# Optimization experiments

Hardware: AMD Instinct MI355X
Metric: run time of the kernel (lower is better)

Reference implementation:

```python
import jax, jax.numpy as jnp
import numpy as np

B, N_E, E_DIM = 131072, 1024, 64
BETA = 0.25


def setup_inputs() -> dict:
    key = jax.random.key(0)
    kz, kw = jax.random.split(key)
    z = jax.random.normal(kz, (B, E_DIM), dtype=jnp.float32)
    # nn.Embedding init: uniform(-1/n_e, 1/n_e)
    emb_w = jax.random.uniform(kw, (N_E, E_DIM), dtype=jnp.float32,
                               minval=-1.0 / N_E, maxval=1.0 / N_E)
    return {"z": z, "emb_w": emb_w}


def reference(z, emb_w):
    beta = jnp.float32(BETA)
    # pairwise squared distances: [B, n_e]
    d = (jnp.sum(z * z, axis=1, keepdims=True)
         + jnp.sum(emb_w * emb_w, axis=1)
         - 2.0 * jnp.einsum('bd,nd->bn', z, emb_w))
    idx = jnp.argmin(d, axis=1)                      # [B]
    z_q = jnp.take(emb_w, idx, axis=0)               # [B, e_dim]
    # legacy=False branch
    loss = (beta * jnp.mean((jax.lax.stop_gradient(z_q) - z) ** 2)
            + jnp.mean((z_q - jax.lax.stop_gradient(z)) ** 2))
    # straight-through estimator
    z_q_st = z + jax.lax.stop_gradient(z_q - z)
    # torch.var is unbiased (ddof=1)
    v = jnp.var(idx.astype(jnp.float32), ddof=1)
    return (z_q_st, loss, idx, v)
```

## Files before the change

### kernel.cpp

```cpp
#include <hip/hip_runtime.h>
#include <stdint.h>


typedef __attribute__((ext_vector_type(8))) __bf16 bf16x8;
typedef __attribute__((ext_vector_type(4))) float f32x4;

#define OUT_LOSS 8388608
#define OUT_IDX  8388609
#define OUT_VAR  8519681

#define WS_LOSS  0
#define WS_S1    4096
#define WS_S2    8192
#define WS_EFRAG 12288
#define WS_EE    143360

__device__ __forceinline__ void gld_lds16(const void* g, void* l) {
  __builtin_amdgcn_global_load_lds(
      (const __attribute__((address_space(1))) unsigned*)g,
      (__attribute__((address_space(3))) unsigned*)l, 16, 0, 0);
}

__global__ void vq_prep(const float* __restrict__ emb, char* __restrict__ ws) {
  bf16x8* efrag = (bf16x8*)(ws + WS_EFRAG);
  float* eeoff = (float*)(ws + WS_EE);
  const int t = blockIdx.x;
  const int l = threadIdx.x;
  const int n = t * 16 + (l & 15);
  const int kb0 = (l >> 4) * 8;
  const float* er = emb + n * 64;
  for (int j = 0; j < 2; ++j) {
    const int kb = j * 32 + kb0;
    bf16x8 h;
#pragma unroll
    for (int i = 0; i < 8; ++i) h[i] = (__bf16)(-2.0f * er[kb + i]);
    efrag[(t * 2 + j) * 64 + l] = h;
  }
  if (l < 16) {
    const float* e2 = emb + (t * 16 + l) * 64;
    float s = 0.f;
#pragma unroll
    for (int d = 0; d < 64; ++d) s += e2[d] * e2[d];
    eeoff[t * 16 + l] = s + 0.5f;
  }
}

__global__ void __launch_bounds__(256) vq_main(
    const float* __restrict__ z, const float* __restrict__ emb,
    float* __restrict__ out, char* __restrict__ ws) {
  __shared__ char smfrag[16384];
  __shared__ float see[1024];
  __shared__ float sL[4];
  __shared__ int sA[4], sB[4];

  const int tid = threadIdx.x;
  const int wave = tid >> 6, lane = tid & 63;
  const int lr = lane & 15, ksl = lane >> 4;
  const int k0 = ksl * 8;
  const int row_base = blockIdx.x * 128 + wave * 32;

  gld_lds16(ws + WS_EE + wave * 1024 + lane * 16, (char*)see + wave * 1024);
#pragma unroll
  for (int i = 0; i < 4; ++i)
    gld_lds16(ws + WS_EFRAG + i * 4096 + wave * 1024 + lane * 16,
              smfrag + i * 4096 + wave * 1024);

  bf16x8 zfa0, zfa1, zfb0, zfb1;
  float zza, zzb;
  {
    const float* zra = z + (size_t)(row_base + lr) * 64;
    const float* zrb = z + (size_t)(row_base + 16 + lr) * 64;
    f32x4 a0 = *(const f32x4*)(zra + k0);
    f32x4 a1 = *(const f32x4*)(zra + k0 + 4);
    f32x4 a2 = *(const f32x4*)(zra + 32 + k0);
    f32x4 a3 = *(const f32x4*)(zra + 32 + k0 + 4);
    f32x4 b0 = *(const f32x4*)(zrb + k0);
    f32x4 b1 = *(const f32x4*)(zrb + k0 + 4);
    f32x4 b2 = *(const f32x4*)(zrb + 32 + k0);
    f32x4 b3 = *(const f32x4*)(zrb + 32 + k0 + 4);
    float sa = 0.f, sb = 0.f;
#pragma unroll
    for (int i = 0; i < 4; ++i) {
      zfa0[i] = (__bf16)a0[i]; zfa0[4 + i] = (__bf16)a1[i];
      zfa1[i] = (__bf16)a2[i]; zfa1[4 + i] = (__bf16)a3[i];
      zfb0[i] = (__bf16)b0[i]; zfb0[4 + i] = (__bf16)b1[i];
      zfb1[i] = (__bf16)b2[i]; zfb1[4 + i] = (__bf16)b3[i];
      sa += a0[i] * a0[i] + a1[i] * a1[i] + a2[i] * a2[i] + a3[i] * a3[i];
      sb += b0[i] * b0[i] + b1[i] * b1[i] + b2[i] * b2[i] + b3[i] * b3[i];
    }
    sa += __shfl_xor(sa, 16, 64); sa += __shfl_xor(sa, 32, 64);
    sb += __shfl_xor(sb, 16, 64); sb += __shfl_xor(sb, 32, 64);
    zza = sa; zzb = sb;
  }

  unsigned rka = 0xFFFFFFFFu, rkb = 0xFFFFFFFFu;
  const unsigned k4 = (unsigned)(ksl * 4);
  const bf16x8* sfrag = (const bf16x8*)smfrag;

  for (int ph = 0; ph < 8; ++ph) {
    __syncthreads();
#pragma unroll
    for (int tt = 0; tt < 8; ++tt) {
      const int g = ph * 8 + tt;
      bf16x8 e0 = sfrag[(tt * 2 + 0) * 64 + lane];
      bf16x8 e1 = sfrag[(tt * 2 + 1) * 64 + lane];
      const f32x4 ee = *(const f32x4*)(see + g * 16 + ksl * 4);
      f32x4 a = __builtin_amdgcn_mfma_f32_16x16x32_bf16(e0, zfa0, ee, 0, 0, 0);
      a = __builtin_amdgcn_mfma_f32_16x16x32_bf16(e1, zfa1, a, 0, 0, 0);
      f32x4 b = __builtin_amdgcn_mfma_f32_16x16x32_bf16(e0, zfb0, ee, 0, 0, 0);
      b = __builtin_amdgcn_mfma_f32_16x16x32_bf16(e1, zfb1, b, 0, 0, 0);
      const unsigned tw = (unsigned)(g * 16);
      {
        const unsigned t0 = (__float_as_uint(a[0]) & 0xFFFFFC00u) | (k4 + 0);
        const unsigned t1 = (__float_as_uint(a[1]) & 0xFFFFFC00u) | (k4 + 1);
        const unsigned t2 = (__float_as_uint(a[2]) & 0xFFFFFC00u) | (k4 + 2);
        const unsigned t3 = (__float_as_uint(a[3]) & 0xFFFFFC00u) | (k4 + 3);
        rka = min(rka, min(min(t0, t1), min(t2, t3)) + tw);
      }
      {
        const unsigned t0 = (__float_as_uint(b[0]) & 0xFFFFFC00u) | (k4 + 0);
        const unsigned t1 = (__float_as_uint(b[1]) & 0xFFFFFC00u) | (k4 + 1);
        const unsigned t2 = (__float_as_uint(b[2]) & 0xFFFFFC00u) | (k4 + 2);
        const unsigned t3 = (__float_as_uint(b[3]) & 0xFFFFFC00u) | (k4 + 3);
        rkb = min(rkb, min(min(t0, t1), min(t2, t3)) + tw);
      }
    }
    __syncthreads();
    if (ph < 7) {
#pragma unroll
      for (int i = 0; i < 4; ++i)
        gld_lds16(ws + WS_EFRAG + (ph + 1) * 16384 + i * 4096 + wave * 1024 + lane * 16,
                  smfrag + i * 4096 + wave * 1024);
    }
  }

  rka = min(rka, (unsigned)__shfl_xor((int)rka, 16, 64));
  rka = min(rka, (unsigned)__shfl_xor((int)rka, 32, 64));
  rkb = min(rkb, (unsigned)__shfl_xor((int)rkb, 16, 64));
  rkb = min(rkb, (unsigned)__shfl_xor((int)rkb, 32, 64));

  const int erow = lane >> 1, eseg = lane & 1;
  const int src = erow & 15;
  const unsigned ka = (unsigned)__shfl((int)rka, src, 64);
  const unsigned kb = (unsigned)__shfl((int)rkb, src, 64);
  const float za = __shfl(zza, src, 64);
  const float zb = __shfl(zzb, src, 64);
  const unsigned k = (erow < 16) ? ka : kb;
  const float zzv = (erow < 16) ? za : zb;
  const unsigned idx = k & 1023u;
  const size_t rowg = (size_t)row_base + erow;
  const f32x4* ep = (const f32x4*)(emb + (size_t)idx * 64 + eseg * 32);
  f32x4* op = (f32x4*)(out + rowg * 64 + eseg * 32);
#pragma unroll
  for (int c = 0; c < 8; ++c) op[c] = ep[c];

  float ls = 0.f; int s1 = 0, s2 = 0;
  if (eseg == 0) {
    ls = zzv + __uint_as_float(k & 0xFFFFFC00u) - 0.5f;
    s1 = (int)idx;
    s2 = (int)(idx * idx);
    out[OUT_IDX + rowg] = (float)idx;
  }
#pragma unroll
  for (int off = 1; off < 64; off <<= 1) {
    ls += __shfl_xor(ls, off, 64);
    s1 += __shfl_xor(s1, off, 64);
    s2 += __shfl_xor(s2, off, 64);
  }
  if (lane == 0) { sL[wave] = ls; sA[wave] = s1; sB[wave] = s2; }
  __syncthreads();
  if (tid == 0) {
    float L = 0; int a = 0, b = 0;
#pragma unroll
    for (int w = 0; w < 4; ++w) { L += sL[w]; a += sA[w]; b += sB[w]; }
    ((float*)(ws + WS_LOSS))[blockIdx.x] = L;
    ((int*)(ws + WS_S1))[blockIdx.x] = a;
    ((int*)(ws + WS_S2))[blockIdx.x] = b;
  }
}

__global__ void vq_final(float* __restrict__ out, const char* __restrict__ ws) {
  const int t = threadIdx.x;
  const float* lp = (const float*)(ws + WS_LOSS);
  const int* p1 = (const int*)(ws + WS_S1);
  const int* p2 = (const int*)(ws + WS_S2);
  double L = 0; long long a = 0, b = 0;
#pragma unroll
  for (int kk = 0; kk < 4; ++kk) {
    const int i = t + 256 * kk;
    L += (double)lp[i];
    a += (long long)p1[i];
    b += (long long)p2[i];
  }
#pragma unroll
  for (int off = 1; off < 64; off <<= 1) {
    L += __shfl_xor(L, off, 64);
    a += __shfl_xor(a, off, 64);
    b += __shfl_xor(b, off, 64);
  }
  __shared__ double sL[4];
  __shared__ long long sA[4], sB[4];
  const int wave = t >> 6, lane = t & 63;
  if (lane == 0) { sL[wave] = L; sA[wave] = a; sB[wave] = b; }
  __syncthreads();
  if (t == 0) {
    double Lt = 0; long long at = 0, bt = 0;
#pragma unroll
    for (int w = 0; w < 4; ++w) { Lt += sL[w]; at += sA[w]; bt += sB[w]; }
    out[OUT_LOSS] = (float)(1.25 * Lt / 8388608.0);
    long long num = bt * 131072LL - at * at;
    out[OUT_VAR] = (float)((double)num / (131072.0 * 131071.0));
  }
}

extern "C" void kernel_launch(void* const* d_in, const int* in_sizes, int n_in,
                              void* d_out, int out_size, void* d_ws, size_t ws_size,
                              hipStream_t stream) {
  (void)in_sizes; (void)n_in; (void)out_size; (void)ws_size;
  const float* z = (const float*)d_in[0];
  const float* emb = (const float*)d_in[1];
  float* out = (float*)d_out;
  char* ws = (char*)d_ws;
  vq_prep<<<64, 64, 0, stream>>>(emb, ws);
  vq_main<<<1024, 256, 0, stream>>>(z, emb, out, ws);
  vq_final<<<1, 256, 0, stream>>>(out, ws);
}
```

Measured before the change: 46.89 us.

## Double-buffer codebook fragments in LDS with explicit vmcnt waits

Splits the LDS fragment buffer into two halves and prefetches the next phase's codebook fragments while the current phase is being computed. Explicit s_waitcnt vmcnt plus raw s_barrier replace the __syncthreads pairs, and the phase loop is fully unrolled. The intent is to hide global-to-LDS load latency behind MFMA work. It also swaps an add for an OR when merging the tile offset into the packed key, which is valid because the low bits are disjoint. The cost is twice the LDS footprint, which may reduce occupancy, and hand-counted vmcnt values that depend on how many loads the compiler has in flight.

Result: faster. 45.70 us (-2.6%).

```diff
diff --git a/kernel.cpp b/kernel.cpp
--- a/kernel.cpp
+++ b/kernel.cpp
@@ -48,7 +48,7 @@
 __global__ void __launch_bounds__(256) vq_main(
     const float* __restrict__ z, const float* __restrict__ emb,
     float* __restrict__ out, char* __restrict__ ws) {
-  __shared__ char smfrag[16384];
+  __shared__ char smfrag[2][16384];
   __shared__ float see[1024];
   __shared__ float sL[4];
   __shared__ int sA[4], sB[4];
@@ -59,11 +59,17 @@
   const int k0 = ksl * 8;
   const int row_base = blockIdx.x * 128 + wave * 32;
 
+#define STAGE(ph, buf)                                                         \
+  {                                                                            \
+    _Pragma("unroll")                                                          \
+    for (int i_ = 0; i_ < 4; ++i_)                                             \
+      gld_lds16(ws + WS_EFRAG + (ph) * 16384 + i_ * 4096 + wave * 1024 + lane * 16, \
+                smfrag[buf] + i_ * 4096 + wave * 1024);                        \
+  }
+
   gld_lds16(ws + WS_EE + wave * 1024 + lane * 16, (char*)see + wave * 1024);
-#pragma unroll
-  for (int i = 0; i < 4; ++i)
-    gld_lds16(ws + WS_EFRAG + i * 4096 + wave * 1024 + lane * 16,
-              smfrag + i * 4096 + wave * 1024);
+  STAGE(0, 0);
+  STAGE(1, 1);
 
   bf16x8 zfa0, zfa1, zfb0, zfb1;
   float zza, zzb;
@@ -95,10 +101,14 @@
 
   unsigned rka = 0xFFFFFFFFu, rkb = 0xFFFFFFFFu;
   const unsigned k4 = (unsigned)(ksl * 4);
-  const bf16x8* sfrag = (const bf16x8*)smfrag;
-
+
+#pragma unroll
   for (int ph = 0; ph < 8; ++ph) {
-    __syncthreads();
+    if (ph < 7) { asm volatile("s_waitcnt vmcnt(4)" ::: "memory"); }
+    else       { asm volatile("s_waitcnt vmcnt(0)" ::: "memory"); }
+    __builtin_amdgcn_sched_barrier(0);
+    __builtin_amdgcn_s_barrier();
+    const bf16x8* sfrag = (const bf16x8*)(smfrag[ph & 1]);
 #pragma unroll
     for (int tt = 0; tt < 8; ++tt) {
       const int g = ph * 8 + tt;
@@ -115,24 +125,20 @@
         const unsigned t1 = (__float_as_uint(a[1]) & 0xFFFFFC00u) | (k4 + 1);
         const unsigned t2 = (__float_as_uint(a[2]) & 0xFFFFFC00u) | (k4 + 2);
         const unsigned t3 = (__float_as_uint(a[3]) & 0xFFFFFC00u) | (k4 + 3);
-        rka = min(rka, min(min(t0, t1), min(t2, t3)) + tw);
+        rka = min(rka, min(min(t0, t1), min(t2, t3)) | tw);
       }
       {
         const unsigned t0 = (__float_as_uint(b[0]) & 0xFFFFFC00u) | (k4 + 0);
         const unsigned t1 = (__float_as_uint(b[1]) & 0xFFFFFC00u) | (k4 + 1);
         const unsigned t2 = (__float_as_uint(b[2]) & 0xFFFFFC00u) | (k4 + 2);
         const unsigned t3 = (__float_as_uint(b[3]) & 0xFFFFFC00u) | (k4 + 3);
-        rkb = min(rkb, min(min(t0, t1), min(t2, t3)) + tw);
+        rkb = min(rkb, min(min(t0, t1), min(t2, t3)) | tw);
       }
     }
-    __syncthreads();
-    if (ph < 7) {
-#pragma unroll
-      for (int i = 0; i < 4; ++i)
-        gld_lds16(ws + WS_EFRAG + (ph + 1) * 16384 + i * 4096 + wave * 1024 + lane * 16,
-                  smfrag + i * 4096 + wave * 1024);
-    }
-  }
+    __builtin_amdgcn_s_barrier();
+    if (ph < 6) STAGE(ph + 2, ph & 1);
+  }
+#undef STAGE
 
   rka = min(rka, (unsigned)__shfl_xor((int)rka, 16, 64));
   rka = min(rka, (unsigned)__shfl_xor((int)rka, 32, 64));
```
